# Kernel optimization log

Measured on AMD Instinct MI355X. Metric: run time of the kernel, lower is better.

## Reference

```python
import jax, jax.numpy as jnp
import numpy as np

D, A, H, FF = 1024, 128, 8, 4096
B, S = 4, 2048
EPS = 1e-5


def setup_inputs() -> dict:
    key = jax.random.key(0)
    ks = jax.random.split(key, 12)
    s = 0.02
    return {
        "x": jax.random.normal(ks[0], (B, S, D), dtype=jnp.float32),
        # per-head QKV projections, stacked over heads: [H, D, A]
        "Wq": jax.random.normal(ks[1], (H, D, A), dtype=jnp.float32) * s,
        "bq": jnp.zeros((H, A), dtype=jnp.float32),
        "Wk": jax.random.normal(ks[2], (H, D, A), dtype=jnp.float32) * s,
        "bk": jnp.zeros((H, A), dtype=jnp.float32),
        "Wv": jax.random.normal(ks[3], (H, D, A), dtype=jnp.float32) * s,
        "bv": jnp.zeros((H, A), dtype=jnp.float32),
        "Wo": jax.random.normal(ks[4], (A, D), dtype=jnp.float32) * s,
        "bo": jnp.zeros((D,), dtype=jnp.float32),
        "g1": jnp.ones((D,), dtype=jnp.float32),
        "beta1": jnp.zeros((D,), dtype=jnp.float32),
        "g2": jnp.ones((D,), dtype=jnp.float32),
        "beta2": jnp.zeros((D,), dtype=jnp.float32),
        "W1": jax.random.normal(ks[5], (D, FF), dtype=jnp.float32) * s,
        "bf1": jnp.zeros((FF,), dtype=jnp.float32),
        "W2": jax.random.normal(ks[6], (FF, D), dtype=jnp.float32) * s,
        "bf2": jnp.zeros((D,), dtype=jnp.float32),
    }


def _layernorm(x, g, b):
    mu = jnp.mean(x, axis=-1, keepdims=True)
    var = jnp.mean(jnp.square(x - mu), axis=-1, keepdims=True)
    return (x - mu) * jax.lax.rsqrt(var + EPS) * g + b


def reference(x, Wq, bq, Wk, bk, Wv, bv, Wo, bo, g1, beta1, g2, beta2, W1, bf1, W2, bf2):
    scale = jnp.sqrt(jnp.float32(A))
    # per-head projections, batched over heads: [H, B, S, A]
    q = jnp.einsum("bsd,hda->hbsa", x, Wq) + bq[:, None, None, :]
    k = jnp.einsum("bsd,hda->hbsa", x, Wk) + bk[:, None, None, :]
    v = jnp.einsum("bsd,hda->hbsa", x, Wv) + bv[:, None, None, :]
    scores = jnp.einsum("hbqa,hbka->hbqk", q, k) / scale  # [H,B,S,S]
    attn = jax.nn.softmax(scores, axis=-1)
    # heads are SUMMED (not concatenated): sum over h -> [B,S,A]
    head_sum = jnp.einsum("hbqk,hbka->bqa", attn, v)
    attn_out = head_sum @ Wo + bo  # [B,S,D]
    x = _layernorm(x + attn_out, g1, beta1)
    h = jax.nn.relu(x @ W1 + bf1)
    ff = h @ W2 + bf2
    return _layernorm(x + ff, g2, beta2)
```

## Files before the change

kernel.cpp:

```cpp
#include <hip/hip_runtime.h>
#include <hip/hip_bf16.h>
#include <stdint.h>

#define DD 1024
#define AA 128
#define HH 8
#define FF 4096
#define BB 4
#define SS 2048
#define MM (BB*SS)
#define EPSV 1e-5f

typedef __bf16 bf16x8 __attribute__((ext_vector_type(8)));
typedef __bf16 bf16x4 __attribute__((ext_vector_type(4)));
typedef float  f32x4  __attribute__((ext_vector_type(4)));
typedef float  f32x16 __attribute__((ext_vector_type(16)));

__device__ __forceinline__ void gload_lds16(const void* g, void* l) {
  __builtin_amdgcn_global_load_lds(
      (const __attribute__((address_space(1))) uint32_t*)(uintptr_t)g,
      (__attribute__((address_space(3))) uint32_t*)(uintptr_t)l, 16, 0, 0);
}

__global__ __launch_bounds__(256) void transpose_conv(const float* __restrict__ in,
                                                      __bf16* __restrict__ out,
                                                      int rows, int cols) {
  __shared__ float tile[64][65];
  const int r0 = blockIdx.y * 64, c0 = blockIdx.x * 64;
  for (int i = threadIdx.x; i < 4096; i += 256) {
    int r = i >> 6, c = i & 63;
    tile[r][c] = in[(long)(r0 + r) * cols + c0 + c];
  }
  __syncthreads();
  for (int i = threadIdx.x; i < 4096; i += 256) {
    int c = i >> 6, r = i & 63;
    out[(long)(c0 + c) * rows + r0 + r] = (__bf16)tile[r][c];
  }
}

__global__ __launch_bounds__(256) void transpose_qkv(const float* __restrict__ Wq,
                                                     const float* __restrict__ Wk,
                                                     const float* __restrict__ Wv,
                                                     __bf16* __restrict__ out) {
  __shared__ float tile[64][65];
  const int z = blockIdx.z;
  const int p = z >> 3, h = z & 7;
  const float* in = ((p == 0) ? Wq : (p == 1) ? Wk : Wv) + (long)h * DD * AA;
  __bf16* o = out + (long)(p * 1024 + h * 128) * DD;
  const int r0 = blockIdx.y * 64, c0 = blockIdx.x * 64;
  for (int i = threadIdx.x; i < 4096; i += 256) {
    int r = i >> 6, c = i & 63;
    tile[r][c] = in[(long)(r0 + r) * AA + c0 + c];
  }
  __syncthreads();
  for (int i = threadIdx.x; i < 4096; i += 256) {
    int c = i >> 6, r = i & 63;
    o[(long)(c0 + c) * DD + r0 + r] = (__bf16)tile[r][c];
  }
}

__global__ __launch_bounds__(256) void transpose_v(const __bf16* __restrict__ qkvb,
                                                   __bf16* __restrict__ vTb) {
  __shared__ float tile[64][65];
  const int s0 = blockIdx.x * 64, a0 = blockIdx.y * 64;
  const int bh = blockIdx.z, b = bh >> 3, h = bh & 7;
  const __bf16* src = qkvb + ((long)b * SS) * 3072 + 2048 + h * 128;
  for (int i = threadIdx.x; i < 4096; i += 256) {
    int r = i >> 6, c = i & 63;
    tile[r][c] = (float)src[(long)(s0 + r) * 3072 + a0 + c];
  }
  __syncthreads();
  __bf16* dst = vTb + ((long)bh * 128) * 2048;
  for (int i = threadIdx.x; i < 4096; i += 256) {
    int c = i >> 6, r = i & 63;
    dst[(long)(a0 + c) * 2048 + s0 + r] = (__bf16)tile[r][c];
  }
}

__global__ void build_qkv_bias(const float* __restrict__ bq, const float* __restrict__ bk,
                               const float* __restrict__ bv, float* __restrict__ out) {
  int i = blockIdx.x * 256 + threadIdx.x;
  if (i < 3072) {
    const float* src = (i < 1024) ? bq : (i < 2048) ? bk : bv;
    out[i] = src[i & 1023];
  }
}

__global__ void conv_f32_bf16(const float* __restrict__ in, __bf16* __restrict__ out, int n4) {
  int i = blockIdx.x * 256 + threadIdx.x;
  if (i < n4) {
    float4 v = ((const float4*)in)[i];
    bf16x4 o = { (__bf16)v.x, (__bf16)v.y, (__bf16)v.z, (__bf16)v.w };
    ((bf16x4*)out)[i] = o;
  }
}

template<bool RELU, bool RESID, bool OUTF, bool OUTB>
__global__ __launch_bounds__(256) void gemm_bt(
    const __bf16* __restrict__ Ag, const __bf16* __restrict__ Bt,
    const float* __restrict__ bias, const float* __restrict__ resid,
    float* __restrict__ Cf, __bf16* __restrict__ Cb,
    int M, int N, int K)
{
  __shared__ __bf16 As[128 * 32];
  __shared__ __bf16 Bs[128 * 32];
  const int t = threadIdx.x;
  const int w = t >> 6, l = t & 63;
  const int gx = gridDim.x, nwg = gx * gridDim.y;
  int bid = blockIdx.y * gx + blockIdx.x;
  int swz = (bid & 7) * (nwg >> 3) + (bid >> 3);
  const int m0 = (swz / gx) * 128, n0 = (swz % gx) * 128;
  const int wr = w >> 1, wc = w & 1;
  const int lr = l & 15, lg = l >> 4;

  f32x4 acc[4][4] = {};

  const __bf16* gA = Ag + (long)(m0 + w * 32 + (l >> 2)) * K + (l & 3) * 8;
  const __bf16* gB = Bt + (long)(n0 + w * 32 + (l >> 2)) * K + (l & 3) * 8;
  __bf16* lA = &As[w * 1024];
  __bf16* lB = &Bs[w * 1024];

  for (int k0 = 0; k0 < K; k0 += 32) {
    gload_lds16(gA + k0, lA);
    gload_lds16(gA + (long)16 * K + k0, lA + 512);
    gload_lds16(gB + k0, lB);
    gload_lds16(gB + (long)16 * K + k0, lB + 512);
    __syncthreads();
    bf16x8 af[4], bfr[4];
#pragma unroll
    for (int mi = 0; mi < 4; mi++)
      af[mi] = *(const bf16x8*)&As[(wr * 64 + mi * 16 + lr) * 32 + lg * 8];
#pragma unroll
    for (int nj = 0; nj < 4; nj++)
      bfr[nj] = *(const bf16x8*)&Bs[(wc * 64 + nj * 16 + lr) * 32 + lg * 8];
#pragma unroll
    for (int mi = 0; mi < 4; mi++)
#pragma unroll
      for (int nj = 0; nj < 4; nj++)
        acc[mi][nj] = __builtin_amdgcn_mfma_f32_16x16x32_bf16(af[mi], bfr[nj], acc[mi][nj], 0, 0, 0);
    __syncthreads();
  }

#pragma unroll
  for (int mi = 0; mi < 4; mi++) {
    const int row0 = m0 + wr * 64 + mi * 16 + lg * 4;
#pragma unroll
    for (int nj = 0; nj < 4; nj++) {
      const int col = n0 + wc * 64 + nj * 16 + lr;
      const float bv = bias[col];
#pragma unroll
      for (int rg = 0; rg < 4; rg++) {
        const int row = row0 + rg;
        float v = acc[mi][nj][rg] + bv;
        if constexpr (RESID) v += resid[(long)row * N + col];
        if constexpr (RELU)  v = fmaxf(v, 0.f);
        if constexpr (OUTF)  Cf[(long)row * N + col] = v;
        if constexpr (OUTB)  Cb[(long)row * N + col] = (__bf16)v;
      }
    }
  }
}

__global__ __launch_bounds__(256) void attn_kernel(
    const __bf16* __restrict__ qkv,
    const __bf16* __restrict__ vT,
    float* __restrict__ hsp)
{
  __shared__ __bf16 Ks[2][64 * 128];
  __shared__ __bf16 Vs[2][128 * 64];
  const int t = threadIdx.x, w = t >> 6, l = t & 63;
  const int q32 = l & 31, hi = l >> 5;
  const int h = blockIdx.y, b = blockIdx.z;
  const long rowbase = (long)b * SS + blockIdx.x * 128 + w * 32;
  const float C2 = (float)(0.08838834764831845 * 1.44269504088896340);

  const __bf16* kbase = qkv + (long)b * SS * 3072 + 1024 + h * 128;
  const __bf16* vbase = vT + ((long)(b * 8 + h) * 128) * 2048;

  bf16x8 qf[8];
  {
    const __bf16* qrow = qkv + (rowbase + q32) * 3072 + h * 128;
#pragma unroll
    for (int ks = 0; ks < 8; ks++) qf[ks] = *(const bf16x8*)(qrow + ks * 16 + hi * 8);
  }

  float mrun = -1e30f, lrun = 0.f;
  f32x16 O[4] = {};

#define STAGE(BUF, KV0)                                                              \
  {                                                                                  \
    _Pragma("unroll")                                                                \
    for (int i = 0; i < 4; i++) {                                                    \
      const int cb = (i * 4 + w) * 64;                                               \
      const int rK = (cb + l) >> 4, cK = l & 15;                                     \
      gload_lds16(kbase + (long)((KV0) + rK) * 3072 + ((cK ^ (rK & 15)) << 3),       \
                  (char*)Ks[BUF] + cb * 16);                                         \
      const int aV = (cb >> 3) + (l >> 3), cV = l & 7;                               \
      gload_lds16(vbase + (long)aV * 2048 + (KV0) + ((cV ^ (aV & 7)) << 3),          \
                  (char*)Vs[BUF] + cb * 16);                                         \
    }                                                                                \
  }

  STAGE(0, 0);
  __syncthreads();
  int cur = 0;

  for (int kt = 0; kt < 32; kt++) {
    if (kt < 31) STAGE(cur ^ 1, (kt + 1) * 64);

    f32x16 st[2] = {};
    __builtin_amdgcn_s_setprio(1);
#pragma unroll
    for (int s2 = 0; s2 < 2; s2++) {
      const int r = s2 * 32 + q32;
#pragma unroll
      for (int ks = 0; ks < 8; ks++) {
        const int g = (2 * ks + hi) ^ (r & 15);
        bf16x8 kf = *(const bf16x8*)((const char*)Ks[cur] + r * 256 + (g << 4));
        st[s2] = __builtin_amdgcn_mfma_f32_32x32x16_bf16(kf, qf[ks], st[s2], 0, 0, 0);
      }
    }
    __builtin_amdgcn_s_setprio(0);

    float pmax = st[0][0];
#pragma unroll
    for (int s2 = 0; s2 < 2; s2++)
#pragma unroll
      for (int rg = 0; rg < 16; rg++) pmax = fmaxf(pmax, st[s2][rg]);
    pmax = fmaxf(pmax, __shfl_xor(pmax, 32));

    if (!__all(pmax - mrun <= 64.f)) {
      const float mnew = fmaxf(mrun, pmax);
      const float sscl = exp2f((mrun - mnew) * C2);
      lrun *= sscl;
      mrun = mnew;
      float ssb[16];
#pragma unroll
      for (int rg = 0; rg < 16; rg++)
        ssb[rg] = __shfl(sscl, (l & 32) + ((rg & 3) + 8 * (rg >> 2) + 4 * hi));
#pragma unroll
      for (int aj = 0; aj < 4; aj++)
#pragma unroll
        for (int rg = 0; rg < 16; rg++) O[aj][rg] *= ssb[rg];
    }

    float rsum = 0.f;
#pragma unroll
    for (int s2 = 0; s2 < 2; s2++)
#pragma unroll
      for (int rg = 0; rg < 16; rg++) {
        const float p = exp2f((st[s2][rg] - mrun) * C2);
        st[s2][rg] = p;
        rsum += p;
      }
    rsum += __shfl_xor(rsum, 32);
    lrun += rsum;

    __builtin_amdgcn_s_setprio(1);
#pragma unroll
    for (int c = 0; c < 4; c++) {
      const int sA = (2 * c) >> 2, tA = (2 * c) & 3;
      const int sB = (2 * c + 1) >> 2, tB = (2 * c + 1) & 3;
      uint32_t W01a, W23a, W01b, W23b;
      asm("v_cvt_pk_bf16_f32 %0, %1, %2" : "=v"(W01a) : "v"(st[sA][4*tA+0]), "v"(st[sA][4*tA+1]));
      asm("v_cvt_pk_bf16_f32 %0, %1, %2" : "=v"(W23a) : "v"(st[sA][4*tA+2]), "v"(st[sA][4*tA+3]));
      asm("v_cvt_pk_bf16_f32 %0, %1, %2" : "=v"(W01b) : "v"(st[sB][4*tB+0]), "v"(st[sB][4*tB+1]));
      asm("v_cvt_pk_bf16_f32 %0, %1, %2" : "=v"(W23b) : "v"(st[sB][4*tB+2]), "v"(st[sB][4*tB+3]));
      const uint32_t X01 = __shfl_xor(hi ? W01a : W01b, 32);
      const uint32_t X23 = __shfl_xor(hi ? W23a : W23b, 32);
      union { uint32_t u[4]; bf16x8 v; } pa;
      pa.u[0] = hi ? X01 : W01a;
      pa.u[1] = hi ? X23 : W23a;
      pa.u[2] = hi ? W01b : X01;
      pa.u[3] = hi ? W23b : X23;
#pragma unroll
      for (int aj = 0; aj < 4; aj++) {
        const int a = aj * 32 + q32;
        const int gv = (2 * c + hi) ^ (a & 7);
        bf16x8 vf = *(const bf16x8*)((const char*)Vs[cur] + a * 128 + (gv << 4));
        O[aj] = __builtin_amdgcn_mfma_f32_32x32x16_bf16(pa.v, vf, O[aj], 0, 0, 0);
      }
    }
    __builtin_amdgcn_s_setprio(0);

    __syncthreads();
    cur ^= 1;
  }
#undef STAGE

  const float invl = 1.f / lrun;
  float invb[16];
#pragma unroll
  for (int rg = 0; rg < 16; rg++)
    invb[rg] = __shfl(invl, (l & 32) + ((rg & 3) + 8 * (rg >> 2) + 4 * hi));
  float* ho = hsp + ((long)h * MM + rowbase) * AA;
#pragma unroll
  for (int aj = 0; aj < 4; aj++)
#pragma unroll
    for (int rg = 0; rg < 16; rg++) {
      const int qr = (rg & 3) + 8 * (rg >> 2) + 4 * hi;
      ho[(long)qr * AA + aj * 32 + q32] = O[aj][rg] * invb[rg];
    }
}

__global__ __launch_bounds__(256) void reduce_heads(const float* __restrict__ hsp,
                                                    __bf16* __restrict__ out) {
  const long i = (long)blockIdx.x * 256 + threadIdx.x;
  const float4* p = (const float4*)hsp;
  float4 s = p[i];
#pragma unroll
  for (int h = 1; h < 8; h++) {
    float4 v = p[i + (long)h * (MM * AA / 4)];
    s.x += v.x; s.y += v.y; s.z += v.z; s.w += v.w;
  }
  bf16x4 o = { (__bf16)s.x, (__bf16)s.y, (__bf16)s.z, (__bf16)s.w };
  ((bf16x4*)out)[i] = o;
}

template<bool WB>
__global__ __launch_bounds__(256) void ln_kernel(
    const float* __restrict__ in, const float* __restrict__ g, const float* __restrict__ be,
    float* __restrict__ outf, __bf16* __restrict__ outb)
{
  const int row = blockIdx.x, t = threadIdx.x;
  const float4 xv = *(const float4*)(in + (long)row * DD + t * 4);
  float s = xv.x + xv.y + xv.z + xv.w;
  float s2 = xv.x * xv.x + xv.y * xv.y + xv.z * xv.z + xv.w * xv.w;
#pragma unroll
  for (int off = 32; off >= 1; off >>= 1) {
    s += __shfl_down(s, off);
    s2 += __shfl_down(s2, off);
  }
  __shared__ float sm[4], sm2[4];
  __shared__ float mu_s, rs_s;
  const int wid = t >> 6;
  if ((t & 63) == 0) { sm[wid] = s; sm2[wid] = s2; }
  __syncthreads();
  if (t == 0) {
    float S = sm[0] + sm[1] + sm[2] + sm[3];
    float S2 = sm2[0] + sm2[1] + sm2[2] + sm2[3];
    float mu = S * (1.f / 1024.f);
    float var = S2 * (1.f / 1024.f) - mu * mu;
    mu_s = mu;
    rs_s = rsqrtf(var + EPSV);
  }
  __syncthreads();
  const float mu = mu_s, rs = rs_s;
  const float4 gv = *(const float4*)(g + t * 4);
  const float4 bv = *(const float4*)(be + t * 4);
  float o0 = (xv.x - mu) * rs * gv.x + bv.x;
  float o1 = (xv.y - mu) * rs * gv.y + bv.y;
  float o2 = (xv.z - mu) * rs * gv.z + bv.z;
  float o3 = (xv.w - mu) * rs * gv.w + bv.w;
  float4 ov = { o0, o1, o2, o3 };
  *(float4*)(outf + (long)row * DD + t * 4) = ov;
  if constexpr (WB) {
    bf16x4 ob = { (__bf16)o0, (__bf16)o1, (__bf16)o2, (__bf16)o3 };
    *(bf16x4*)(outb + (long)row * DD + t * 4) = ob;
  }
}

extern "C" void kernel_launch(void* const* d_in, const int* in_sizes, int n_in,
                              void* d_out, int out_size, void* d_ws, size_t ws_size,
                              hipStream_t stream) {
  const float* x    = (const float*)d_in[0];
  const float* Wq   = (const float*)d_in[1];
  const float* bq   = (const float*)d_in[2];
  const float* Wk   = (const float*)d_in[3];
  const float* bk   = (const float*)d_in[4];
  const float* Wv   = (const float*)d_in[5];
  const float* bv   = (const float*)d_in[6];
  const float* Wo   = (const float*)d_in[7];
  const float* bo   = (const float*)d_in[8];
  const float* g1   = (const float*)d_in[9];
  const float* be1  = (const float*)d_in[10];
  const float* g2   = (const float*)d_in[11];
  const float* be2  = (const float*)d_in[12];
  const float* W1   = (const float*)d_in[13];
  const float* bf1  = (const float*)d_in[14];
  const float* W2   = (const float*)d_in[15];
  const float* bf2  = (const float*)d_in[16];

  const size_t MB = 1ull << 20;
  char* ws = (char*)d_ws;
  __bf16* WqkvT    = (__bf16*)(ws + 0);
  float*  qkv_bias = (float*) (ws + 6 * MB);
  __bf16* WoT      = (__bf16*)(ws + 7 * MB);
  __bf16* W1T      = (__bf16*)(ws + 8 * MB);
  __bf16* W2T      = (__bf16*)(ws + 16 * MB);
  __bf16* xb       = (__bf16*)(ws + 24 * MB);
  __bf16* qkvb     = (__bf16*)(ws + 40 * MB);
  __bf16* vTb      = (__bf16*)(ws + 88 * MB);
  float*  hsp      = (float*) (ws + 104 * MB);
  __bf16* hs_b     = (__bf16*)(ws + 136 * MB);
  float*  tt       = (float*) (ws + 104 * MB);
  float*  yy       = (float*) (ws + 140 * MB);
  __bf16* yb       = (__bf16*)(ws + 172 * MB);
  __bf16* hb       = (__bf16*)(ws + 24 * MB);

  transpose_qkv<<<dim3(2, 16, 24), 256, 0, stream>>>(Wq, Wk, Wv, WqkvT);
  build_qkv_bias<<<12, 256, 0, stream>>>(bq, bk, bv, qkv_bias);
  transpose_conv<<<dim3(16, 2), 256, 0, stream>>>(Wo, WoT, 128, 1024);
  transpose_conv<<<dim3(64, 16), 256, 0, stream>>>(W1, W1T, 1024, 4096);
  transpose_conv<<<dim3(16, 64), 256, 0, stream>>>(W2, W2T, 4096, 1024);
  conv_f32_bf16<<<8192, 256, 0, stream>>>(x, xb, MM * DD / 4);

  gemm_bt<false, false, false, true><<<dim3(24, 64), 256, 0, stream>>>(
      xb, WqkvT, qkv_bias, nullptr, nullptr, qkvb, MM, 3072, 1024);
  transpose_v<<<dim3(32, 2, 32), 256, 0, stream>>>(qkvb, vTb);

  attn_kernel<<<dim3(16, 8, 4), 256, 0, stream>>>(qkvb, vTb, hsp);
  reduce_heads<<<MM * AA / 4 / 256, 256, 0, stream>>>(hsp, hs_b);

  gemm_bt<false, true, true, false><<<dim3(8, 64), 256, 0, stream>>>(
      hs_b, WoT, bo, x, tt, nullptr, MM, 1024, 128);
  ln_kernel<true><<<MM, 256, 0, stream>>>(tt, g1, be1, yy, yb);

  gemm_bt<true, false, false, true><<<dim3(32, 64), 256, 0, stream>>>(
      yb, W1T, bf1, nullptr, nullptr, hb, MM, FF, 1024);
  gemm_bt<false, true, true, false><<<dim3(8, 64), 256, 0, stream>>>(
      hb, W2T, bf2, yy, tt, nullptr, MM, DD, FF);
  ln_kernel<false><<<MM, 256, 0, stream>>>(tt, g2, be2, (float*)d_out, nullptr);
}
```

Measured before the change: 610.0 us.

## Add 256x256-tile pipelined GEMM for QKV and FFN1 projections

```diff
diff --git a/kernel.cpp b/kernel.cpp
--- a/kernel.cpp
+++ b/kernel.cpp
@@ -156,6 +156,134 @@
         if constexpr (RELU)  v = fmaxf(v, 0.f);
         if constexpr (OUTF)  Cf[(long)row * N + col] = v;
         if constexpr (OUTB)  Cb[(long)row * N + col] = (__bf16)v;
+      }
+    }
+  }
+}
+
+template<bool RELU>
+__global__ __launch_bounds__(512, 2) void gemm256(
+    const __bf16* __restrict__ Ag, const __bf16* __restrict__ Bt,
+    const float* __restrict__ bias, __bf16* __restrict__ Cb,
+    int M, int N, int K)
+{
+  __shared__ __bf16 As[2][256 * 64];
+  __shared__ __bf16 Bs[2][256 * 64];
+  const int t = threadIdx.x, w = t >> 6, l = t & 63;
+  const int gx = gridDim.x, nwg = gx * gridDim.y;
+  int bid = blockIdx.y * gx + blockIdx.x;
+  int swz = (bid & 7) * (nwg >> 3) + (bid >> 3);
+  const int m0 = (swz / gx) * 256, n0 = (swz % gx) * 256;
+  const int wr = w >> 2, wc = w & 3;
+  const int lr = l & 15, lg = l >> 4;
+  const int NK = K / 64;
+
+  f32x4 acc[8][4] = {};
+
+  const int srow = l >> 3;
+  const int sg = l & 7;
+
+#define STAGE_A(BUF, KT, HALF)                                                          \
+  {                                                                                     \
+    _Pragma("unroll")                                                                   \
+    for (int j = 0; j < 2; j++) {                                                       \
+      const int r0 = (HALF) * 128 + w * 16 + j * 8;                                     \
+      const int r = r0 + srow;                                                          \
+      const int gs = sg ^ (r & 7);                                                      \
+      gload_lds16(Ag + (long)(m0 + r) * K + (KT) * 64 + gs * 8,                         \
+                  (char*)As[BUF] + r0 * 128);                                           \
+    }                                                                                   \
+  }
+#define STAGE_B(BUF, KT, HALF)                                                          \
+  {                                                                                     \
+    _Pragma("unroll")                                                                   \
+    for (int j = 0; j < 2; j++) {                                                       \
+      const int r0 = (HALF) * 128 + w * 16 + j * 8;                                     \
+      const int r = r0 + srow;                                                          \
+      const int gs = sg ^ (r & 7);                                                      \
+      gload_lds16(Bt + (long)(n0 + r) * K + (KT) * 64 + gs * 8,                         \
+                  (char*)Bs[BUF] + r0 * 128);                                           \
+    }                                                                                   \
+  }
+
+  STAGE_A(0, 0, 0); STAGE_A(0, 0, 1);
+  STAGE_B(0, 0, 0); STAGE_B(0, 0, 1);
+  STAGE_B(1, 1, 0); STAGE_B(1, 1, 1);
+  asm volatile("s_waitcnt vmcnt(4)" ::: "memory");
+  __builtin_amdgcn_sched_barrier(0);
+  __builtin_amdgcn_s_barrier();
+
+  for (int kt = 0; kt < NK; kt++) {
+    const int c = kt & 1, nb = c ^ 1;
+    const char* Ab = (const char*)As[c];
+    const char* Bb = (const char*)Bs[c];
+    bf16x8 bfr[4][2];
+    bf16x8 af[2][2];
+
+#pragma unroll
+    for (int ph = 0; ph < 4; ph++) {
+      if (ph == 0) { if (kt + 1 < NK) STAGE_A(nb, kt + 1, 0); }
+      if (ph == 1) {
+        if (kt + 1 < NK) STAGE_A(nb, kt + 1, 1);
+        if (kt + 2 < NK) STAGE_B(c, kt + 2, 0);
+      }
+      if (ph == 2) { if (kt + 2 < NK) STAGE_B(c, kt + 2, 1); }
+
+      if (ph == 0) {
+#pragma unroll
+        for (int nj = 0; nj < 4; nj++)
+#pragma unroll
+          for (int kh = 0; kh < 2; kh++) {
+            const int r = wc * 64 + nj * 16 + lr;
+            bfr[nj][kh] = *(const bf16x8*)(Bb + r * 128 + (((kh * 4 + lg) ^ (r & 7)) << 4));
+          }
+      }
+#pragma unroll
+      for (int mi2 = 0; mi2 < 2; mi2++)
+#pragma unroll
+        for (int kh = 0; kh < 2; kh++) {
+          const int r = wr * 128 + (ph * 2 + mi2) * 16 + lr;
+          af[mi2][kh] = *(const bf16x8*)(Ab + r * 128 + (((kh * 4 + lg) ^ (r & 7)) << 4));
+        }
+
+      asm volatile("s_waitcnt lgkmcnt(0)" ::: "memory");
+      __builtin_amdgcn_sched_barrier(0);
+
+      __builtin_amdgcn_s_setprio(1);
+#pragma unroll
+      for (int mi2 = 0; mi2 < 2; mi2++) {
+        const int mi = ph * 2 + mi2;
+#pragma unroll
+        for (int nj = 0; nj < 4; nj++)
+#pragma unroll
+          for (int kh = 0; kh < 2; kh++)
+            acc[mi][nj] = __builtin_amdgcn_mfma_f32_16x16x32_bf16(af[mi2][kh], bfr[nj][kh],
+                                                                  acc[mi][nj], 0, 0, 0);
+      }
+      __builtin_amdgcn_s_setprio(0);
+
+      if (ph == 3) {
+        asm volatile("s_waitcnt vmcnt(4)" ::: "memory");
+        __builtin_amdgcn_sched_barrier(0);
+      }
+      __builtin_amdgcn_s_barrier();
+    }
+  }
+#undef STAGE_A
+#undef STAGE_B
+
+#pragma unroll
+  for (int mi = 0; mi < 8; mi++) {
+    const int row0 = m0 + wr * 128 + mi * 16 + lg * 4;
+#pragma unroll
+    for (int nj = 0; nj < 4; nj++) {
+      const int col = n0 + wc * 64 + nj * 16 + lr;
+      const float bv = bias[col];
+#pragma unroll
+      for (int rg = 0; rg < 4; rg++) {
+        float v = acc[mi][nj][rg] + bv;
+        if constexpr (RELU) v = fmaxf(v, 0.f);
+        Cb[(long)(row0 + rg) * N + col] = (__bf16)v;
       }
     }
   }
@@ -405,8 +533,8 @@
   transpose_conv<<<dim3(16, 64), 256, 0, stream>>>(W2, W2T, 4096, 1024);
   conv_f32_bf16<<<8192, 256, 0, stream>>>(x, xb, MM * DD / 4);
 
-  gemm_bt<false, false, false, true><<<dim3(24, 64), 256, 0, stream>>>(
-      xb, WqkvT, qkv_bias, nullptr, nullptr, qkvb, MM, 3072, 1024);
+  gemm256<false><<<dim3(12, 32), 512, 0, stream>>>(
+      xb, WqkvT, qkv_bias, qkvb, MM, 3072, 1024);
   transpose_v<<<dim3(32, 2, 32), 256, 0, stream>>>(qkvb, vTb);
 
   attn_kernel<<<dim3(16, 8, 4), 256, 0, stream>>>(qkvb, vTb, hsp);
@@ -416,8 +544,8 @@
       hs_b, WoT, bo, x, tt, nullptr, MM, 1024, 128);
   ln_kernel<true><<<MM, 256, 0, stream>>>(tt, g1, be1, yy, yb);
 
-  gemm_bt<true, false, false, true><<<dim3(32, 64), 256, 0, stream>>>(
-      yb, W1T, bf1, nullptr, nullptr, hb, MM, FF, 1024);
+  gemm256<true><<<dim3(16, 32), 512, 0, stream>>>(
+      yb, W1T, bf1, hb, MM, FF, 1024);
   gemm_bt<false, true, true, false><<<dim3(8, 64), 256, 0, stream>>>(
       hb, W2T, bf2, yy, tt, nullptr, MM, DD, FF);
   ln_kernel<false><<<MM, 256, 0, stream>>>(tt, g2, be2, (float*)d_out, nullptr);
```

Result: faster. 597.9 us (-2.0%).
